# Kernel tuning notes

Hardware: AMD Instinct MI355X
Metric: run time of the kernel (lower is better)

## Reference

```python
import jax, jax.numpy as jnp
import numpy as np

# ---- static config (from init_kwargs) ----
B, H, W, C = 4, 256, 256, 96
WS, SS, NH = 8, 4, 3            # window_size, shift_size, num_heads
N = WS * WS                     # tokens per window = 64
NW = (H // WS) * (W // WS)      # windows per image = 1024
HD = C // NH                    # head_dim = 32
SCALE = HD ** -0.5
MLP_H = int(C * 4.0)
EPS = 1e-5


def _relative_position_index():
    coords = np.stack(np.meshgrid(np.arange(WS), np.arange(WS), indexing='ij'))  # (2, WS, WS)
    cf = coords.reshape(2, -1)                       # (2, N)
    rel = (cf[:, :, None] - cf[:, None, :]).transpose(1, 2, 0).astype(np.int64)  # (N, N, 2)
    rel[:, :, 0] += WS - 1
    rel[:, :, 1] += WS - 1
    rel[:, :, 0] *= 2 * WS - 1
    return rel.sum(-1)                               # (N, N) in [0, (2WS-1)^2)


def _attn_mask():
    img = np.zeros((H, W))
    cnt = 0
    slices = (slice(0, -WS), slice(-WS, -SS), slice(-SS, None))
    for hs in slices:
        for ws in slices:
            img[hs, ws] = cnt
            cnt += 1
    m = img.reshape(H // WS, WS, W // WS, WS).transpose(0, 2, 1, 3).reshape(-1, N)  # (NW, N)
    am = m[:, None, :] - m[:, :, None]               # (NW, N, N)
    return np.where(am != 0, -100.0, 0.0).astype(np.float32)


def setup_inputs() -> dict:
    key = jax.random.key(0)
    ks = jax.random.split(key, 8)
    std = 0.02
    inp = {
        'x': jax.random.normal(ks[0], (B, H * W, C), jnp.float32),
        'g1': jnp.ones((C,), jnp.float32),
        'b1': jnp.zeros((C,), jnp.float32),
        'qkv_w': jax.random.normal(ks[1], (3 * C, C), jnp.float32) * std,
        'qkv_b': jnp.zeros((3 * C,), jnp.float32),
        'rpb_table': jax.random.normal(ks[2], ((2 * WS - 1) ** 2, NH), jnp.float32) * std,
        'proj_w': jax.random.normal(ks[3], (C, C), jnp.float32) * std,
        'proj_b': jnp.zeros((C,), jnp.float32),
        'g2': jnp.ones((C,), jnp.float32),
        'b2': jnp.zeros((C,), jnp.float32),
        'fc1_w': jax.random.normal(ks[4], (MLP_H, C), jnp.float32) * std,
        'fc1_b': jnp.zeros((MLP_H,), jnp.float32),
        'fc2_w': jax.random.normal(ks[5], (C, MLP_H), jnp.float32) * std,
        'fc2_b': jnp.zeros((C,), jnp.float32),
        'attn_mask': jnp.asarray(_attn_mask()),
        'rel_index': jnp.asarray(_relative_position_index(), jnp.int32),
    }
    return inp


def _ln(x, g, b):
    mu = jnp.mean(x, -1, keepdims=True)
    var = jnp.mean(jnp.square(x - mu), -1, keepdims=True)
    return (x - mu) * jax.lax.rsqrt(var + EPS) * g + b


def reference(x, g1, b1, qkv_w, qkv_b, rpb_table, proj_w, proj_b,
              g2, b2, fc1_w, fc1_b, fc2_w, fc2_b, attn_mask, rel_index):
    shortcut = x
    h = _ln(x, g1, b1).reshape(B, H, W, C)
    # cyclic shift
    h = jnp.roll(h, (-SS, -SS), axis=(1, 2))
    # window partition -> (B*NW, N, C)
    xw = h.reshape(B, H // WS, WS, W // WS, WS, C).transpose(0, 1, 3, 2, 4, 5).reshape(-1, N, C)
    # qkv projection
    qkv = (xw @ qkv_w.T + qkv_b).reshape(-1, N, 3, NH, HD).transpose(2, 0, 3, 1, 4)  # (3, B_, NH, N, HD)
    q, k, v = qkv[0] * SCALE, qkv[1], qkv[2]
    attn = jnp.einsum('bhnd,bhmd->bhnm', q, k)       # (B_, NH, N, N)
    # gathered relative position bias: (N, N, NH) -> (NH, N, N)
    bias = rpb_table[rel_index].transpose(2, 0, 1)
    attn = attn + bias[None]
    # shifted-window mask
    attn = attn.reshape(B, NW, NH, N, N) + attn_mask[None, :, None]
    attn = jax.nn.softmax(attn.reshape(-1, NH, N, N), axis=-1)
    o = jnp.einsum('bhnm,bhmd->bhnd', attn, v).transpose(0, 2, 1, 3).reshape(-1, N, C)
    o = o @ proj_w.T + proj_b
    # window reverse + reverse shift
    o = o.reshape(B, H // WS, W // WS, WS, WS, C).transpose(0, 1, 3, 2, 4, 5).reshape(B, H, W, C)
    o = jnp.roll(o, (SS, SS), axis=(1, 2)).reshape(B, H * W, C)
    x = shortcut + o
    h2 = _ln(x, g2, b2)
    h2 = jax.nn.gelu(h2 @ fc1_w.T + fc1_b, approximate=False) @ fc2_w.T + fc2_b
    return x + h2
```

## Files before the change

### kernel.cpp

```cpp
#include <hip/hip_runtime.h>
#include <hip/hip_bf16.h>
#include <math.h>

constexpr float SCALE_ = 0.17677669529663687f;

typedef float f32x4 __attribute__((ext_vector_type(4)));
typedef short bf16x8 __attribute__((ext_vector_type(8)));
typedef short short4v __attribute__((ext_vector_type(4)));
#define MFMA __builtin_amdgcn_mfma_f32_16x16x32_bf16


__device__ inline short f2bf(float f) {
    __hip_bfloat16 h = __float2bfloat16(f);
    return *reinterpret_cast<short*>(&h);
}
__device__ inline float bf2f(short s) {
    union { unsigned u; float f; } v; v.u = ((unsigned)(unsigned short)s) << 16;
    return v.f;
}
__device__ inline float gelu_erf(float v) {
    float z  = v * 0.70710678f;
    float z2 = fminf(z * z, 1.5f);
    float p  =      0.00012055333f;
    p = p * z2 -    0.00085483270f;
    p = p * z2 +    0.0052239776f;
    p = p * z2 -    0.0268661706f;
    p = p * z2 +    0.1128379167f;
    p = p * z2 -    0.3761263890f;
    p = p * z2 +    1.1283791671f;
    float er = z * p;
    float t  = 0.5f * v;
    return t * er + t;
}

__global__ __launch_bounds__(256)
void prep_weights(const float* __restrict__ qkv_w, const float* __restrict__ proj_w,
                  const float* __restrict__ fc1_w, const float* __restrict__ fc2_w,
                  short* __restrict__ ws)
{
    int i = blockIdx.x * 256 + threadIdx.x;
    if (i >= 110592) return;
    float v;
    if      (i < 27648)  v = qkv_w[i];
    else if (i < 36864)  v = proj_w[i - 27648];
    else if (i < 73728)  v = fc1_w[i - 36864];
    else                 v = fc2_w[i - 73728];
    ws[i] = f2bf(v);
}

__global__ __launch_bounds__(256)
void prep_comb(const float* __restrict__ rpb, const int* __restrict__ rel,
               const float* __restrict__ mask, short* __restrict__ comb)
{
    int e = blockIdx.x * 256 + threadIdx.x;
    if (e >= 49152) return;
    int t   = e / 12288;
    int rem = e - t * 12288;
    int h   = rem >> 12;
    int ij  = rem & 4095;
    const int rep[4] = {0, 31, 992, 1023};
    comb[e] = f2bf(rpb[rel[ij] * 3 + h] + mask[(long)rep[t] * 4096 + ij]);
}

__global__ __launch_bounds__(256, 3)
void attn_kernel(const float* __restrict__ x,
                 const float* __restrict__ g1, const float* __restrict__ b1,
                 const short* __restrict__ qkv_wb, const float* __restrict__ qkv_b,
                 const short* __restrict__ proj_wb, const float* __restrict__ proj_b,
                 const short* __restrict__ comb,
                 float* __restrict__ xnew)
{
    __shared__ short aL[64][104];
    __shared__ short qpL[64][104];
    __shared__ short kL[64][104];
    __shared__ short vT[96][72];

    const int tid  = threadIdx.x;
    const int wave = tid >> 6, lane = tid & 63;
    const int lr = lane & 15, lg = lane >> 4;
    const int blk = blockIdx.x;
    const int b = blk >> 10, wi = blk & 1023;
    const int wh = wi >> 5, ww = wi & 31;
    const int mtyp = ((wh == 31) ? 2 : 0) + ((ww == 31) ? 1 : 0);

    auto tok_of = [&](int n) -> int {
        int r = n >> 3, c = n & 7;
        int gh = (wh * 8 + r + 4) & 255;
        int gw = (ww * 8 + c + 4) & 255;
        return b * 65536 + gh * 256 + gw;
    };

    {
        const int n = tid >> 2, s = tid & 3;
        const float* xr = x + (long)tok_of(n) * 96 + s * 24;
        float xv[24];
        #pragma unroll
        for (int i = 0; i < 6; i++) {
            float4 t = ((const float4*)xr)[i];
            xv[4*i]=t.x; xv[4*i+1]=t.y; xv[4*i+2]=t.z; xv[4*i+3]=t.w;
        }
        float s1 = 0.f, s2 = 0.f;
        #pragma unroll
        for (int i = 0; i < 24; i++) { s1 += xv[i]; s2 += xv[i]*xv[i]; }
        s1 += __shfl_xor(s1, 1); s2 += __shfl_xor(s2, 1);
        s1 += __shfl_xor(s1, 2); s2 += __shfl_xor(s2, 2);
        float mu = s1 * (1.0f/96.0f);
        float var = s2 * (1.0f/96.0f) - mu*mu;
        float rs = rsqrtf(var + 1e-5f);
        #pragma unroll
        for (int c = 0; c < 24; c++)
            aL[n][s*24+c] = f2bf((xv[c]-mu)*rs*g1[s*24+c] + b1[s*24+c]);
    }
    __syncthreads();

    {
        const int wm = wave >> 1, wn = wave & 1;
        bf16x8 afr[2][3];
        #pragma unroll
        for (int mt = 0; mt < 2; mt++)
            #pragma unroll
            for (int kt = 0; kt < 3; kt++)
                afr[mt][kt] = *(const bf16x8*)&aL[(2*wm+mt)*16 + lr][kt*32 + lg*8];
        for (int nt0 = 0; nt0 < 9; nt0++) {
            const int nt = wn * 9 + nt0;
            const int o  = nt * 16 + lr;
            bf16x8 bfr[3];
            #pragma unroll
            for (int kt = 0; kt < 3; kt++)
                bfr[kt] = *(const bf16x8*)&qkv_wb[(long)o * 96 + kt*32 + lg*8];
            const float bias = qkv_b[o];
            #pragma unroll
            for (int mt = 0; mt < 2; mt++) {
                f32x4 acc = {bias, bias, bias, bias};
                #pragma unroll
                for (int kt = 0; kt < 3; kt++)
                    acc = MFMA(afr[mt][kt], bfr[kt], acc, 0, 0, 0);
                const int row0 = (2*wm+mt)*16 + lg*4;
                if (nt < 6) {
                    #pragma unroll
                    for (int r = 0; r < 4; r++) qpL[row0+r][o] = f2bf(acc[r]*SCALE_);
                } else if (nt < 12) {
                    #pragma unroll
                    for (int r = 0; r < 4; r++) kL[row0+r][o-96] = f2bf(acc[r]);
                } else {
                    #pragma unroll
                    for (int r = 0; r < 4; r++) vT[o-192][row0+r] = f2bf(acc[r]);
                }
            }
        }
    }
    __syncthreads();

    bf16x8 qf[3];
    #pragma unroll
    for (int h = 0; h < 3; h++)
        qf[h] = *(const bf16x8*)&qpL[wave*16 + lr][h*32 + lg*8];

    for (int h = 0; h < 3; h++) {
        const short* cb = comb + (mtyp * 3 + h) * 4096;
        float sv[4][4];
        #pragma unroll
        for (int nt = 0; nt < 4; nt++) {
            bf16x8 kf = *(const bf16x8*)&kL[nt*16 + lr][h*32 + lg*8];
            f32x4 s = MFMA(qf[h], kf, (f32x4){0.f,0.f,0.f,0.f}, 0, 0, 0);
            #pragma unroll
            for (int r = 0; r < 4; r++) {
                int i = wave*16 + lg*4 + r;
                int j = nt*16 + lr;
                sv[nt][r] = s[r] + bf2f(cb[i*64 + j]);
            }
        }
        float mx[4], sm[4];
        #pragma unroll
        for (int r = 0; r < 4; r++) {
            mx[r] = fmaxf(fmaxf(sv[0][r], sv[1][r]), fmaxf(sv[2][r], sv[3][r]));
            mx[r] = fmaxf(mx[r], __shfl_xor(mx[r], 1));
            mx[r] = fmaxf(mx[r], __shfl_xor(mx[r], 2));
            mx[r] = fmaxf(mx[r], __shfl_xor(mx[r], 4));
            mx[r] = fmaxf(mx[r], __shfl_xor(mx[r], 8));
            sm[r] = 0.f;
        }
        #pragma unroll
        for (int nt = 0; nt < 4; nt++)
            #pragma unroll
            for (int r = 0; r < 4; r++) { sv[nt][r] = __expf(sv[nt][r]-mx[r]); sm[r] += sv[nt][r]; }
        #pragma unroll
        for (int r = 0; r < 4; r++) {
            sm[r] += __shfl_xor(sm[r], 1);
            sm[r] += __shfl_xor(sm[r], 2);
            sm[r] += __shfl_xor(sm[r], 4);
            sm[r] += __shfl_xor(sm[r], 8);
            sm[r] = 1.0f / sm[r];
        }
        #pragma unroll
        for (int nt = 0; nt < 4; nt++)
            #pragma unroll
            for (int r = 0; r < 4; r++)
                qpL[wave*16 + lg*4 + r][nt*16 + lr] = f2bf(sv[nt][r]*sm[r]);

        bf16x8 pf[2];
        #pragma unroll
        for (int kt = 0; kt < 2; kt++)
            pf[kt] = *(const bf16x8*)&qpL[wave*16 + lr][kt*32 + lg*8];
        #pragma unroll
        for (int nt = 0; nt < 2; nt++) {
            f32x4 acc = {0.f,0.f,0.f,0.f};
            #pragma unroll
            for (int kt = 0; kt < 2; kt++) {
                bf16x8 vf = *(const bf16x8*)&vT[h*32 + nt*16 + lr][kt*32 + lg*8];
                acc = MFMA(pf[kt], vf, acc, 0, 0, 0);
            }
            #pragma unroll
            for (int r = 0; r < 4; r++)
                aL[wave*16 + lg*4 + r][h*32 + nt*16 + lr] = f2bf(acc[r]);
        }
    }
    __syncthreads();

    {
        const int wm = wave >> 1, wn = wave & 1;
        bf16x8 afr[2][3];
        #pragma unroll
        for (int mt = 0; mt < 2; mt++)
            #pragma unroll
            for (int kt = 0; kt < 3; kt++)
                afr[mt][kt] = *(const bf16x8*)&aL[(2*wm+mt)*16 + lr][kt*32 + lg*8];
        for (int nt0 = 0; nt0 < 3; nt0++) {
            const int nt = wn * 3 + nt0;
            const int c  = nt * 16 + lr;
            bf16x8 bfr[3];
            #pragma unroll
            for (int kt = 0; kt < 3; kt++)
                bfr[kt] = *(const bf16x8*)&proj_wb[(long)c * 96 + kt*32 + lg*8];
            const float bias = proj_b[c];
            #pragma unroll
            for (int mt = 0; mt < 2; mt++) {
                f32x4 acc = {bias, bias, bias, bias};
                #pragma unroll
                for (int kt = 0; kt < 3; kt++)
                    acc = MFMA(afr[mt][kt], bfr[kt], acc, 0, 0, 0);
                #pragma unroll
                for (int r = 0; r < 4; r++) {
                    int i = (2*wm+mt)*16 + lg*4 + r;
                    long ad = (long)tok_of(i) * 96 + c;
                    xnew[ad] = acc[r] + x[ad];
                }
            }
        }
    }
}

__global__ __launch_bounds__(256, 4)
void mlp_kernel(const float* __restrict__ g2, const float* __restrict__ b2,
                const short* __restrict__ fc1_wb, const float* __restrict__ fc1_b,
                const short* __restrict__ fc2_wb, const float* __restrict__ fc2_b,
                float* __restrict__ xio)
{
    __shared__ short smem[9216];
    short (*aL)[104]    = (short(*)[104])smem;
    short (*hch)[64][72] = (short(*)[64][72])smem;

    const int tid  = threadIdx.x;
    const int wave = tid >> 6, lane = tid & 63;
    const int lr = lane & 15, lg = lane >> 4;
    const int wm = wave >> 1, wn = wave & 1;
    const long base = (long)blockIdx.x * 6144;

    {
        const int n = tid >> 2, s = tid & 3;
        const float* xr = xio + base + n * 96 + s * 24;
        float xv[24];
        #pragma unroll
        for (int i = 0; i < 6; i++) {
            float4 t = ((const float4*)xr)[i];
            xv[4*i]=t.x; xv[4*i+1]=t.y; xv[4*i+2]=t.z; xv[4*i+3]=t.w;
        }
        float s1 = 0.f, s2 = 0.f;
        #pragma unroll
        for (int i = 0; i < 24; i++) { s1 += xv[i]; s2 += xv[i]*xv[i]; }
        s1 += __shfl_xor(s1, 1); s2 += __shfl_xor(s2, 1);
        s1 += __shfl_xor(s1, 2); s2 += __shfl_xor(s2, 2);
        float mu  = s1 * (1.0f/96.0f);
        float var = s2 * (1.0f/96.0f) - mu*mu;
        float rs  = rsqrtf(var + 1e-5f);
        #pragma unroll
        for (int j = 0; j < 12; j++) {
            const int ch = s*24 + 2*j;
            unsigned lo = (unsigned short)f2bf((xv[2*j  ]-mu)*rs*g2[ch  ] + b2[ch  ]);
            unsigned hi = (unsigned short)f2bf((xv[2*j+1]-mu)*rs*g2[ch+1] + b2[ch+1]);
            *(unsigned*)&aL[n][ch] = lo | (hi << 16);
        }
    }
    __syncthreads();

    bf16x8 bx[2][3];
    #pragma unroll
    for (int tt = 0; tt < 2; tt++)
        #pragma unroll
        for (int kt = 0; kt < 3; kt++)
            bx[tt][kt] = *(const bf16x8*)&aL[(wn*2+tt)*16 + lr][kt*32 + lg*8];
    __syncthreads();

    f32x4 facc[3][2];
    #pragma unroll
    for (int nt = 0; nt < 3; nt++) {
        const float4 bb = *(const float4*)&fc2_b[(wm*3+nt)*16 + lg*4];
        facc[nt][0] = (f32x4){bb.x, bb.y, bb.z, bb.w};
        facc[nt][1] = facc[nt][0];
    }

    for (int c = 0; c < 6; c++) {
        const int cbuf = c & 1;
        f32x4 acc1[2][2];
        #pragma unroll
        for (int h2 = 0; h2 < 2; h2++) {
            const int ht = wm*2 + h2;
            const int o  = c*64 + ht*16 + lr;
            bf16x8 wfr[3];
            #pragma unroll
            for (int kt = 0; kt < 3; kt++)
                wfr[kt] = *(const bf16x8*)&fc1_wb[(long)o * 96 + kt*32 + lg*8];
            const float4 bi = *(const float4*)&fc1_b[c*64 + ht*16 + lg*4];
            const f32x4 binit = {bi.x, bi.y, bi.z, bi.w};
            #pragma unroll
            for (int tt = 0; tt < 2; tt++) {
                f32x4 acc = binit;
                #pragma unroll
                for (int kt = 0; kt < 3; kt++)
                    acc = MFMA(wfr[kt], bx[tt][kt], acc, 0, 0, 0);
                acc1[h2][tt] = acc;
            }
        }
        #pragma unroll
        for (int h2 = 0; h2 < 2; h2++)
            #pragma unroll
            for (int tt = 0; tt < 2; tt++) {
                short4v sv;
                #pragma unroll
                for (int r = 0; r < 4; r++)
                    sv[r] = f2bf(gelu_erf(acc1[h2][tt][r]));
                const int tok = (wn*2+tt)*16 + lr;
                const int hid = (wm*2+h2)*16 + lg*4;
                *(short4v*)&hch[cbuf][tok][hid] = sv;
            }
        __syncthreads();
        #pragma unroll
        for (int tt = 0; tt < 2; tt++) {
            bf16x8 hf[2];
            #pragma unroll
            for (int kt = 0; kt < 2; kt++)
                hf[kt] = *(const bf16x8*)&hch[cbuf][(wn*2+tt)*16 + lr][kt*32 + lg*8];
            #pragma unroll
            for (int nt = 0; nt < 3; nt++) {
                #pragma unroll
                for (int kt = 0; kt < 2; kt++) {
                    bf16x8 wf2 = *(const bf16x8*)&fc2_wb[(long)((wm*3+nt)*16 + lr) * 384 + c*64 + kt*32 + lg*8];
                    facc[nt][tt] = MFMA(wf2, hf[kt], facc[nt][tt], 0, 0, 0);
                }
            }
        }
    }

    #pragma unroll
    for (int nt = 0; nt < 3; nt++)
        #pragma unroll
        for (int tt = 0; tt < 2; tt++) {
            const int tok  = (wn*2+tt)*16 + lr;
            const int ocol = (wm*3+nt)*16 + lg*4;
            const long ad  = base + (long)tok * 96 + ocol;
            float4 o = *(const float4*)&xio[ad];
            o.x += facc[nt][tt][0]; o.y += facc[nt][tt][1];
            o.z += facc[nt][tt][2]; o.w += facc[nt][tt][3];
            *(float4*)&xio[ad] = o;
        }
}

extern "C" void kernel_launch(void* const* d_in, const int* in_sizes, int n_in,
                              void* d_out, int out_size, void* d_ws, size_t ws_size,
                              hipStream_t stream)
{
    const float* x      = (const float*)d_in[0];
    const float* g1     = (const float*)d_in[1];
    const float* b1     = (const float*)d_in[2];
    const float* qkv_w  = (const float*)d_in[3];
    const float* qkv_b  = (const float*)d_in[4];
    const float* rpb    = (const float*)d_in[5];
    const float* proj_w = (const float*)d_in[6];
    const float* proj_b = (const float*)d_in[7];
    const float* g2     = (const float*)d_in[8];
    const float* b2     = (const float*)d_in[9];
    const float* fc1_w  = (const float*)d_in[10];
    const float* fc1_b  = (const float*)d_in[11];
    const float* fc2_w  = (const float*)d_in[12];
    const float* fc2_b  = (const float*)d_in[13];
    const float* mask   = (const float*)d_in[14];
    const int*   rel    = (const int*)d_in[15];
    float* out = (float*)d_out;

    short* wsS    = (short*)d_ws;
    short* qkv_wb = wsS;
    short* proj_wb= wsS + 27648;
    short* fc1_wb = wsS + 36864;
    short* fc2_wb = wsS + 73728;
    short* comb   = wsS + 110592;

    prep_weights<<<432, 256, 0, stream>>>(qkv_w, proj_w, fc1_w, fc2_w, wsS);
    prep_comb<<<192, 256, 0, stream>>>(rpb, rel, mask, comb);
    attn_kernel<<<4096, 256, 0, stream>>>(x, g1, b1, qkv_wb, qkv_b,
                                          proj_wb, proj_b, comb, out);
    mlp_kernel<<<4096, 256, 0, stream>>>(g2, b2, fc1_wb, fc1_b, fc2_wb, fc2_b, out);
}
```

Before: 240.0 us.

## Transpose attention MFMAs for row-per-lane softmax and prefetch MLP weights

Swaps the MFMA operand order in the QK^T and PV products so each lane holds a query row's contiguous columns. Softmax max and sum reductions then need two cross-lane shuffles instead of four per row, and results are written to LDS as packed 64-bit bf16 stores instead of scalar shorts. The bias table is read as a vector load. In the MLP loop, fc1 weights for the next chunk are prefetched during the current chunk and fc2 weights are loaded before the barrier, to hide global-load latency at the cost of more registers.

```diff
diff --git a/kernel.cpp b/kernel.cpp
--- a/kernel.cpp
+++ b/kernel.cpp
@@ -17,6 +17,10 @@
 __device__ inline float bf2f(short s) {
     union { unsigned u; float f; } v; v.u = ((unsigned)(unsigned short)s) << 16;
     return v.f;
+}
+__device__ inline unsigned pack2bf(float lo, float hi) {
+    return (unsigned)(unsigned short)f2bf(lo) |
+           ((unsigned)(unsigned short)f2bf(hi) << 16);
 }
 __device__ inline float gelu_erf(float v) {
     float z  = v * 0.70710678f;
@@ -108,8 +112,12 @@
         float var = s2 * (1.0f/96.0f) - mu*mu;
         float rs = rsqrtf(var + 1e-5f);
         #pragma unroll
-        for (int c = 0; c < 24; c++)
-            aL[n][s*24+c] = f2bf((xv[c]-mu)*rs*g1[s*24+c] + b1[s*24+c]);
+        for (int c = 0; c < 12; c++) {
+            const int ch = s*24 + 2*c;
+            *(unsigned*)&aL[n][ch] =
+                pack2bf((xv[2*c  ]-mu)*rs*g1[ch  ] + b1[ch  ],
+                        (xv[2*c+1]-mu)*rs*g1[ch+1] + b1[ch+1]);
+        }
     }
     __syncthreads();
 
@@ -162,41 +170,34 @@
         #pragma unroll
         for (int nt = 0; nt < 4; nt++) {
             bf16x8 kf = *(const bf16x8*)&kL[nt*16 + lr][h*32 + lg*8];
-            f32x4 s = MFMA(qf[h], kf, (f32x4){0.f,0.f,0.f,0.f}, 0, 0, 0);
-            #pragma unroll
-            for (int r = 0; r < 4; r++) {
-                int i = wave*16 + lg*4 + r;
-                int j = nt*16 + lr;
-                sv[nt][r] = s[r] + bf2f(cb[i*64 + j]);
-            }
-        }
-        float mx[4], sm[4];
-        #pragma unroll
-        for (int r = 0; r < 4; r++) {
-            mx[r] = fmaxf(fmaxf(sv[0][r], sv[1][r]), fmaxf(sv[2][r], sv[3][r]));
-            mx[r] = fmaxf(mx[r], __shfl_xor(mx[r], 1));
-            mx[r] = fmaxf(mx[r], __shfl_xor(mx[r], 2));
-            mx[r] = fmaxf(mx[r], __shfl_xor(mx[r], 4));
-            mx[r] = fmaxf(mx[r], __shfl_xor(mx[r], 8));
-            sm[r] = 0.f;
-        }
+            f32x4 s = MFMA(kf, qf[h], (f32x4){0.f,0.f,0.f,0.f}, 0, 0, 0);
+            short4v bb = *(const short4v*)&cb[(wave*16 + lr)*64 + nt*16 + lg*4];
+            #pragma unroll
+            for (int r = 0; r < 4; r++)
+                sv[nt][r] = s[r] + bf2f(bb[r]);
+        }
+        float m = sv[0][0];
         #pragma unroll
         for (int nt = 0; nt < 4; nt++)
             #pragma unroll
-            for (int r = 0; r < 4; r++) { sv[nt][r] = __expf(sv[nt][r]-mx[r]); sm[r] += sv[nt][r]; }
-        #pragma unroll
-        for (int r = 0; r < 4; r++) {
-            sm[r] += __shfl_xor(sm[r], 1);
-            sm[r] += __shfl_xor(sm[r], 2);
-            sm[r] += __shfl_xor(sm[r], 4);
-            sm[r] += __shfl_xor(sm[r], 8);
-            sm[r] = 1.0f / sm[r];
-        }
+            for (int r = 0; r < 4; r++) m = fmaxf(m, sv[nt][r]);
+        m = fmaxf(m, __shfl_xor(m, 16));
+        m = fmaxf(m, __shfl_xor(m, 32));
+        float sum = 0.f;
         #pragma unroll
         for (int nt = 0; nt < 4; nt++)
             #pragma unroll
-            for (int r = 0; r < 4; r++)
-                qpL[wave*16 + lg*4 + r][nt*16 + lr] = f2bf(sv[nt][r]*sm[r]);
+            for (int r = 0; r < 4; r++) { sv[nt][r] = __expf(sv[nt][r]-m); sum += sv[nt][r]; }
+        sum += __shfl_xor(sum, 16);
+        sum += __shfl_xor(sum, 32);
+        const float inv = 1.0f / sum;
+        #pragma unroll
+        for (int nt = 0; nt < 4; nt++) {
+            uint2 w;
+            w.x = pack2bf(sv[nt][0]*inv, sv[nt][1]*inv);
+            w.y = pack2bf(sv[nt][2]*inv, sv[nt][3]*inv);
+            *(uint2*)&qpL[wave*16 + lr][nt*16 + lg*4] = w;
+        }
 
         bf16x8 pf[2];
         #pragma unroll
@@ -208,11 +209,12 @@
             #pragma unroll
             for (int kt = 0; kt < 2; kt++) {
                 bf16x8 vf = *(const bf16x8*)&vT[h*32 + nt*16 + lr][kt*32 + lg*8];
-                acc = MFMA(pf[kt], vf, acc, 0, 0, 0);
-            }
-            #pragma unroll
-            for (int r = 0; r < 4; r++)
-                aL[wave*16 + lg*4 + r][h*32 + nt*16 + lr] = f2bf(acc[r]);
+                acc = MFMA(vf, pf[kt], acc, 0, 0, 0);
+            }
+            uint2 w;
+            w.x = pack2bf(acc[0], acc[1]);
+            w.y = pack2bf(acc[2], acc[3]);
+            *(uint2*)&aL[wave*16 + lr][h*32 + nt*16 + lg*4] = w;
         }
     }
     __syncthreads();
@@ -286,9 +288,9 @@
         #pragma unroll
         for (int j = 0; j < 12; j++) {
             const int ch = s*24 + 2*j;
-            unsigned lo = (unsigned short)f2bf((xv[2*j  ]-mu)*rs*g2[ch  ] + b2[ch  ]);
-            unsigned hi = (unsigned short)f2bf((xv[2*j+1]-mu)*rs*g2[ch+1] + b2[ch+1]);
-            *(unsigned*)&aL[n][ch] = lo | (hi << 16);
+            *(unsigned*)&aL[n][ch] =
+                pack2bf((xv[2*j  ]-mu)*rs*g2[ch  ] + b2[ch  ],
+                        (xv[2*j+1]-mu)*rs*g2[ch+1] + b2[ch+1]);
         }
     }
     __syncthreads();
@@ -309,39 +311,58 @@
         facc[nt][1] = facc[nt][0];
     }
 
+    bf16x8 wfrA[2][3];
+    f32x4  biA[2];
+    #pragma unroll
+    for (int h2 = 0; h2 < 2; h2++) {
+        const int o = (wm*2+h2)*16 + lr;
+        #pragma unroll
+        for (int kt = 0; kt < 3; kt++)
+            wfrA[h2][kt] = *(const bf16x8*)&fc1_wb[(long)o * 96 + kt*32 + lg*8];
+        const float4 bi = *(const float4*)&fc1_b[(wm*2+h2)*16 + lg*4];
+        biA[h2] = (f32x4){bi.x, bi.y, bi.z, bi.w};
+    }
+
     for (int c = 0; c < 6; c++) {
         const int cbuf = c & 1;
+        bf16x8 wf2[3][2];
+        #pragma unroll
+        for (int nt = 0; nt < 3; nt++)
+            #pragma unroll
+            for (int kt = 0; kt < 2; kt++)
+                wf2[nt][kt] = *(const bf16x8*)&fc2_wb[(long)((wm*3+nt)*16 + lr) * 384 + c*64 + kt*32 + lg*8];
         f32x4 acc1[2][2];
         #pragma unroll
-        for (int h2 = 0; h2 < 2; h2++) {
-            const int ht = wm*2 + h2;
-            const int o  = c*64 + ht*16 + lr;
-            bf16x8 wfr[3];
-            #pragma unroll
-            for (int kt = 0; kt < 3; kt++)
-                wfr[kt] = *(const bf16x8*)&fc1_wb[(long)o * 96 + kt*32 + lg*8];
-            const float4 bi = *(const float4*)&fc1_b[c*64 + ht*16 + lg*4];
-            const f32x4 binit = {bi.x, bi.y, bi.z, bi.w};
+        for (int h2 = 0; h2 < 2; h2++)
             #pragma unroll
             for (int tt = 0; tt < 2; tt++) {
-                f32x4 acc = binit;
+                f32x4 acc = biA[h2];
                 #pragma unroll
                 for (int kt = 0; kt < 3; kt++)
-                    acc = MFMA(wfr[kt], bx[tt][kt], acc, 0, 0, 0);
+                    acc = MFMA(wfrA[h2][kt], bx[tt][kt], acc, 0, 0, 0);
                 acc1[h2][tt] = acc;
             }
+        if (c < 5) {
+            #pragma unroll
+            for (int h2 = 0; h2 < 2; h2++) {
+                const int o = (c+1)*64 + (wm*2+h2)*16 + lr;
+                #pragma unroll
+                for (int kt = 0; kt < 3; kt++)
+                    wfrA[h2][kt] = *(const bf16x8*)&fc1_wb[(long)o * 96 + kt*32 + lg*8];
+                const float4 bi = *(const float4*)&fc1_b[(c+1)*64 + (wm*2+h2)*16 + lg*4];
+                biA[h2] = (f32x4){bi.x, bi.y, bi.z, bi.w};
+            }
         }
         #pragma unroll
         for (int h2 = 0; h2 < 2; h2++)
             #pragma unroll
             for (int tt = 0; tt < 2; tt++) {
-                short4v sv;
-                #pragma unroll
-                for (int r = 0; r < 4; r++)
-                    sv[r] = f2bf(gelu_erf(acc1[h2][tt][r]));
+                uint2 w;
+                w.x = pack2bf(gelu_erf(acc1[h2][tt][0]), gelu_erf(acc1[h2][tt][1]));
+                w.y = pack2bf(gelu_erf(acc1[h2][tt][2]), gelu_erf(acc1[h2][tt][3]));
                 const int tok = (wn*2+tt)*16 + lr;
                 const int hid = (wm*2+h2)*16 + lg*4;
-                *(short4v*)&hch[cbuf][tok][hid] = sv;
+                *(uint2*)&hch[cbuf][tok][hid] = w;
             }
         __syncthreads();
         #pragma unroll
@@ -351,13 +372,10 @@
             for (int kt = 0; kt < 2; kt++)
                 hf[kt] = *(const bf16x8*)&hch[cbuf][(wn*2+tt)*16 + lr][kt*32 + lg*8];
             #pragma unroll
-            for (int nt = 0; nt < 3; nt++) {
-                #pragma unroll
-                for (int kt = 0; kt < 2; kt++) {
-                    bf16x8 wf2 = *(const bf16x8*)&fc2_wb[(long)((wm*3+nt)*16 + lr) * 384 + c*64 + kt*32 + lg*8];
-                    facc[nt][tt] = MFMA(wf2, hf[kt], facc[nt][tt], 0, 0, 0);
-                }
-            }
+            for (int nt = 0; nt < 3; nt++)
+                #pragma unroll
+                for (int kt = 0; kt < 2; kt++)
+                    facc[nt][tt] = MFMA(wf2[nt][kt], hf[kt], facc[nt][tt], 0, 0, 0);
         }
     }
 
```

Measured after the change: 233.2 us. 1.03x faster.
